# Kernel optimization log

Hardware: AMD Instinct MI355X
Metric: run time of the kernel (lower is better)

The kernel has to match this reference:

```python
import jax, jax.numpy as jnp
import numpy as np

B, S, D, H = 4, 2048, 1024, 16
DK = D // H
NEG = -1.0e9

def setup_inputs() -> dict:
    key = jax.random.key(0)
    ks = jax.random.split(key, 9)
    scale = 1.0 / np.sqrt(D)
    x = jax.random.normal(ks[0], (B, S, D), dtype=jnp.float32)
    # causal mask: positions with mask==0 are filled with -1e9
    mask = jnp.tril(jnp.ones((S, S), dtype=jnp.int32))[None, None]  # [1,1,S,S]
    Wq = jax.random.normal(ks[1], (D, D), dtype=jnp.float32) * scale
    bq = jax.random.normal(ks[2], (D,), dtype=jnp.float32) * 0.01
    Wk = jax.random.normal(ks[3], (D, D), dtype=jnp.float32) * scale
    bk = jax.random.normal(ks[4], (D,), dtype=jnp.float32) * 0.01
    Wv = jax.random.normal(ks[5], (D, D), dtype=jnp.float32) * scale
    bv = jax.random.normal(ks[6], (D,), dtype=jnp.float32) * 0.01
    Wo = jax.random.normal(ks[7], (D, D), dtype=jnp.float32) * scale
    bo = jax.random.normal(ks[8], (D,), dtype=jnp.float32) * 0.01
    return {"x": x, "mask": mask, "Wq": Wq, "bq": bq, "Wk": Wk, "bk": bk,
            "Wv": Wv, "bv": bv, "Wo": Wo, "bo": bo}

def reference(x, mask, Wq, bq, Wk, bk, Wv, bv, Wo, bo):
    Bb, Ss, Dd = x.shape
    q = (x @ Wq.T + bq).reshape(Bb, Ss, H, DK).transpose(0, 2, 1, 3)  # [B,H,S,DK]
    k = (x @ Wk.T + bk).reshape(Bb, Ss, H, DK).transpose(0, 2, 1, 3)
    v = (x @ Wv.T + bv).reshape(Bb, Ss, H, DK).transpose(0, 2, 1, 3)
    scaled = jnp.einsum('bhqd,bhkd->bhqk', q, k) / jnp.sqrt(jnp.float32(DK))
    scaled = jnp.where(mask == 0, jnp.float32(NEG), scaled)
    attn = jax.nn.softmax(scaled, axis=-1)  # dropout prob = 0 -> identity
    vals = jnp.einsum('bhqk,bhkd->bhqd', attn, v)  # [B,H,S,DK]
    vals = vals.transpose(0, 2, 1, 3).reshape(Bb, Ss, H * DK)
    out = vals @ Wo.T + bo
    return out
```

## Files before the change

kernel.cpp:

```cpp
#include <hip/hip_runtime.h>
#include <hip/hip_bf16.h>
#include <cstdint>

#define B_ 4
#define S_ 2048
#define D_ 1024
#define H_ 16
#define DK_ 64

typedef _Float16 h8 __attribute__((ext_vector_type(8)));
typedef _Float16 h4 __attribute__((ext_vector_type(4)));
typedef float f32x4 __attribute__((ext_vector_type(4)));
typedef float f32x16 __attribute__((ext_vector_type(16)));
typedef unsigned int u32x4 __attribute__((ext_vector_type(4)));

__device__ __forceinline__ void gload16(const void* src, void* lds) {
  __builtin_amdgcn_global_load_lds((const __attribute__((address_space(1))) void*)src,
                                   (__attribute__((address_space(3))) void*)lds, 16, 0, 0);
}

__global__ __launch_bounds__(256) void conv_all(
    const float* __restrict__ x,
    const float* __restrict__ Wq, const float* __restrict__ Wk,
    const float* __restrict__ Wv, const float* __restrict__ Wo,
    const float* __restrict__ bq, const float* __restrict__ bk,
    const float* __restrict__ bv,
    _Float16* __restrict__ xb, _Float16* __restrict__ wqkv,
    _Float16* __restrict__ wo, float* __restrict__ bqkv) {
  const int bid = blockIdx.x, tid = threadIdx.x;
  if (bid < 4096) {
    int base = (bid * 256 + tid) * 8;
    h8 o;
#pragma unroll
    for (int j = 0; j < 8; ++j) o[j] = (_Float16)x[base + j];
    *(h8*)(xb + base) = o;
  } else {
    int i = (bid - 4096) * 256 + tid;
    int seg = i >> 17, r = i & 131071;
    const float* src = seg == 0 ? Wq : seg == 1 ? Wk : seg == 2 ? Wv : Wo;
    int base = r * 8;
    h8 o;
#pragma unroll
    for (int j = 0; j < 8; ++j) o[j] = (_Float16)src[base + j];
    if (seg < 3)
      *(h8*)(wqkv + (size_t)seg * 1048576 + base) = o;
    else
      *(h8*)(wo + base) = o;
    if (i < 768) {
      int bsel = i >> 8, k = (i & 255) * 4;
      const float* bs = bsel == 0 ? bq : bsel == 1 ? bk : bv;
      float4 v = *(const float4*)(bs + k);
      *(float4*)(bqkv + bsel * 1024 + k) = v;
    }
  }
}

template <int MODE>
__global__ __launch_bounds__(256, 2) void gemm_nt(const _Float16* __restrict__ A,
                                                  const _Float16* __restrict__ Bw,
                                                  const float* __restrict__ bias,
                                                  void* __restrict__ Cout,
                                                  _Float16* __restrict__ Vt) {
  __shared__ char lds[49152];

  const int tid = threadIdx.x;
  const int w = tid >> 6, lane = tid & 63, g = lane >> 4, c = lane & 15;
  const int wm = w >> 1, wn = w & 1;
  const int bn = blockIdx.x;
  const int bm = blockIdx.y;

  f32x4 acc[8][4] = {};

  const int srow = tid >> 3;
  const int scolsw = ((tid & 7) * 16) ^ ((srow & 7) << 4);
  const char* Ab = (const char*)A + (size_t)bm * 256 * 2048;
  const char* Bb = (const char*)Bw + (size_t)bn * 128 * 2048;
  const char* Asrc[8];
  const char* Bsrc[4];
#pragma unroll
  for (int j = 0; j < 8; ++j)
    Asrc[j] = Ab + (size_t)(j * 32 + srow) * 2048 + scolsw;
#pragma unroll
  for (int j = 0; j < 4; ++j)
    Bsrc[j] = Bb + (size_t)(j * 32 + srow) * 2048 + scolsw;
  char* dstA = lds + w * 1024;
  char* dstB = lds + 32768 + w * 1024;

  for (int k0 = 0; k0 < 2048; k0 += 128) {
    __syncthreads();
#pragma unroll
    for (int j = 0; j < 8; ++j) gload16(Asrc[j] + k0, dstA + j * 4096);
#pragma unroll
    for (int j = 0; j < 4; ++j) gload16(Bsrc[j] + k0, dstB + j * 4096);
    __syncthreads();

#pragma unroll
    for (int kk = 0; kk < 2; ++kk) {
      h8 b[4];
#pragma unroll
      for (int ni = 0; ni < 4; ++ni) {
        int row = wn * 64 + ni * 16 + c;
        int off = row * 128 + kk * 64 + g * 16;
        b[ni] = *(const h8*)(lds + 32768 + (off ^ ((row & 7) << 4)));
      }
      h8 a[8];
#pragma unroll
      for (int mi = 0; mi < 8; ++mi) {
        int row = wm * 128 + mi * 16 + c;
        int off = row * 128 + kk * 64 + g * 16;
        a[mi] = *(const h8*)(lds + (off ^ ((row & 7) << 4)));
      }
      __builtin_amdgcn_s_setprio(1);
#pragma unroll
      for (int mi = 0; mi < 8; ++mi)
#pragma unroll
        for (int ni = 0; ni < 4; ++ni)
          acc[mi][ni] = __builtin_amdgcn_mfma_f32_16x16x32_f16(a[mi], b[ni], acc[mi][ni], 0, 0, 0);
      __builtin_amdgcn_s_setprio(0);
    }
  }

  if (MODE == 0 && bn >= 16) {
#pragma unroll
    for (int mi = 0; mi < 8; ++mi)
#pragma unroll
      for (int ni = 0; ni < 4; ++ni) {
        int m0 = bm * 256 + wm * 128 + mi * 16 + g * 4;
        int n = bn * 128 + wn * 64 + ni * 16 + c;
        float bb = bias[n];
        h4 v4;
#pragma unroll
        for (int r = 0; r < 4; ++r) v4[r] = (_Float16)(acc[mi][ni][r] + bb);
        int bI = m0 >> 11, sI = m0 & 2047;
        int dk = n & 63, hh = (n >> 6) & 15;
        *(h4*)(Vt + (((size_t)(bI * 16 + hh) * 64 + dk) * 2048 + sI)) = v4;
      }
  } else {
#pragma unroll
    for (int mi = 0; mi < 8; ++mi)
#pragma unroll
      for (int ni = 0; ni < 4; ++ni)
#pragma unroll
        for (int r = 0; r < 4; ++r) {
          int m = bm * 256 + wm * 128 + mi * 16 + g * 4 + r;
          int n = bn * 128 + wn * 64 + ni * 16 + c;
          float v = acc[mi][ni][r] + bias[n];
          if (MODE == 0) {
            int which = n >> 10, nn = n & 1023;
            int bI = m >> 11, sI = m & 2047, hI = nn >> 6, dkI = nn & 63;
            ((_Float16*)Cout)[(size_t)which * 8388608 +
                              (((size_t)bI * H_ + hI) * S_ + sI) * DK_ + dkI] = (_Float16)v;
          } else {
            ((float*)Cout)[(size_t)m * D_ + n] = v;
          }
        }
  }
}

__global__ __launch_bounds__(512) void attn_fwd(const _Float16* __restrict__ Q,
                                                const _Float16* __restrict__ K,
                                                const _Float16* __restrict__ Vt,
                                                _Float16* __restrict__ vals) {
  __shared__ char lds[3 * 16384];

  const int tid = threadIdx.x;
  const int w = tid >> 6;
  const int lane = tid & 63;
  const int l31 = lane & 31, hi = lane >> 5;
  const int bid = blockIdx.x;
  const int pi = bid >> 6;
  const int bh = bid & 63;
  const int bI = bh >> 4, hI = bh & 15;

  const char* Qb = (const char*)(Q + (size_t)bh * S_ * DK_);
  const char* Kb = (const char*)(K + (size_t)bh * S_ * DK_);
  const char* Vtb = (const char*)(Vt + (size_t)bh * DK_ * S_);

  auto stage = [&](int sloti, int kv0) {
    char* buf = lds + sloti * 16384;
    gload16(Kb + (size_t)kv0 * 128 + (size_t)lane * 128 + w * 16, buf + w * 1024);
    gload16(Vtb + (size_t)lane * 4096 + (size_t)kv0 * 2 + w * 16, buf + 8192 + w * 1024);
  };

  int rdo[4];
#pragma unroll
  for (int ks = 0; ks < 4; ++ks) rdo[ks] = (ks * 2 + hi) * 1024 + l31 * 16;

  const _Float16 qsc = (_Float16)(0.125f * 1.44269504f);

  for (int phase = 0; phase < 2; ++phase) {
    const int sup = (phase == 0) ? pi : 7 - pi;
    const int qw = sup * 8 + w;
    const int nt = 4 * sup + 4;

    h8 qf[4];
#pragma unroll
    for (int ks = 0; ks < 4; ++ks) {
      h8 v = *(const h8*)(Qb + (size_t)(qw * 32 + l31) * 128 + ks * 32 + hi * 16);
#pragma unroll
      for (int j = 0; j < 8; ++j) v[j] *= qsc;
      qf[ks] = v;
    }

    f32x16 o[2] = {};
    float m_ = -1e30f, l_ = 0.f;

    stage(0, 0);
    stage(1, 64);
    asm volatile("s_waitcnt vmcnt(2)" ::: "memory");
    __builtin_amdgcn_s_barrier();
    asm volatile("" ::: "memory");

    for (int t = 0; t < nt; ++t) {
      const char* ldsb = lds + (t % 3) * 16384;
      if (t + 2 < nt) stage((t + 2) % 3, (t + 2) * 64);

      const int rel = qw - 2 * t;
      if (rel >= 0) {
        const bool have1 = (rel >= 1);

        f32x16 s0 = {}, s1 = {};
#pragma unroll
        for (int ks = 0; ks < 4; ++ks) {
          h8 k0 = *(const h8*)(ldsb + rdo[ks]);
          __builtin_amdgcn_s_setprio(1);
          s0 = __builtin_amdgcn_mfma_f32_32x32x16_f16(k0, qf[ks], s0, 0, 0, 0);
          __builtin_amdgcn_s_setprio(0);
          if (have1) {
            h8 k1 = *(const h8*)(ldsb + rdo[ks] + 512);
            __builtin_amdgcn_s_setprio(1);
            s1 = __builtin_amdgcn_mfma_f32_32x32x16_f16(k1, qf[ks], s1, 0, 0, 0);
            __builtin_amdgcn_s_setprio(0);
          }
        }

        if (rel == 0) {
#pragma unroll
          for (int r = 0; r < 16; ++r) {
            int rowidx = (r & 3) + 8 * (r >> 2) + 4 * hi;
            if (rowidx > l31) s0[r] = -1e30f;
          }
        } else if (rel == 1) {
#pragma unroll
          for (int r = 0; r < 16; ++r) {
            int rowidx = (r & 3) + 8 * (r >> 2) + 4 * hi;
            if (rowidx > l31) s1[r] = -1e30f;
          }
        }

        float t8[8];
#pragma unroll
        for (int j = 0; j < 8; ++j) t8[j] = fmaxf(s0[2 * j], s0[2 * j + 1]);
        if (have1)
#pragma unroll
          for (int j = 0; j < 8; ++j) t8[j] = fmaxf(t8[j], fmaxf(s1[2 * j], s1[2 * j + 1]));
        float t4a = fmaxf(t8[0], t8[1]), t4b = fmaxf(t8[2], t8[3]);
        float t4c = fmaxf(t8[4], t8[5]), t4d = fmaxf(t8[6], t8[7]);
        float pmax = fmaxf(fmaxf(t4a, t4b), fmaxf(t4c, t4d));

        if (!__all(pmax <= m_ + 8.f)) {
          float rm = fmaxf(pmax, __shfl_xor(pmax, 32));
          float mn = fmaxf(m_, rm);
          float al = __builtin_amdgcn_exp2f(m_ - mn);
          m_ = mn;
          l_ *= al;
#pragma unroll
          for (int r = 0; r < 16; ++r) {
            float av = __shfl(al, (r & 3) + 8 * (r >> 2) + 4 * hi);
            o[0][r] *= av;
            o[1][r] *= av;
          }
        }

        unsigned int u0[8], u1[8];
        float rsa = 0.f, rsb = 0.f;
#pragma unroll
        for (int j = 0; j < 8; ++j) {
          float e0 = __builtin_amdgcn_exp2f(s0[2 * j] - m_);
          float e1 = __builtin_amdgcn_exp2f(s0[2 * j + 1] - m_);
          rsa += e0 + e1;
          u0[j] = __builtin_bit_cast(unsigned int, __builtin_amdgcn_cvt_pkrtz(e0, e1));
        }
        if (have1) {
#pragma unroll
          for (int j = 0; j < 8; ++j) {
            float e0 = __builtin_amdgcn_exp2f(s1[2 * j] - m_);
            float e1 = __builtin_amdgcn_exp2f(s1[2 * j + 1] - m_);
            rsb += e0 + e1;
            u1[j] = __builtin_bit_cast(unsigned int, __builtin_amdgcn_cvt_pkrtz(e0, e1));
          }
        }
        l_ += rsa + rsb;

        h8 pa0[2], pa1[2];
#pragma unroll
        for (int b = 0; b < 2; ++b) {
          unsigned int ua = u0[4 * b], ub = u0[4 * b + 1];
          unsigned int uc = u0[4 * b + 2], ud = u0[4 * b + 3];
          unsigned int va = hi ? ua : uc, vb = hi ? ub : ud;
          unsigned int xa = __shfl_xor(va, 32), xb = __shfl_xor(vb, 32);
          u32x4 q = {hi ? xa : ua, hi ? xb : ub, hi ? uc : xa, hi ? ud : xb};
          pa0[b] = __builtin_bit_cast(h8, q);
        }
        if (have1) {
#pragma unroll
          for (int b = 0; b < 2; ++b) {
            unsigned int ua = u1[4 * b], ub = u1[4 * b + 1];
            unsigned int uc = u1[4 * b + 2], ud = u1[4 * b + 3];
            unsigned int va = hi ? ua : uc, vb = hi ? ub : ud;
            unsigned int xa = __shfl_xor(va, 32), xb = __shfl_xor(vb, 32);
            u32x4 q = {hi ? xa : ua, hi ? xb : ub, hi ? uc : xa, hi ? ud : xb};
            pa1[b] = __builtin_bit_cast(h8, q);
          }
        }

#pragma unroll
        for (int x = 0; x < 2; ++x) {
#pragma unroll
          for (int kvs = 0; kvs < 4; ++kvs) {
            int ni = kvs >> 1, b = kvs & 1;
            if (!have1 && ni == 1) continue;
            h8 vf = *(const h8*)(ldsb + 8192 + rdo[kvs] + x * 512);
            h8 pa = ni ? pa1[b] : pa0[b];
            __builtin_amdgcn_s_setprio(1);
            o[x] = __builtin_amdgcn_mfma_f32_32x32x16_f16(pa, vf, o[x], 0, 0, 0);
            __builtin_amdgcn_s_setprio(0);
          }
        }
      }

      if (t + 2 < nt)
        asm volatile("s_waitcnt vmcnt(2)" ::: "memory");
      else
        asm volatile("s_waitcnt vmcnt(0)" ::: "memory");
      __builtin_amdgcn_s_barrier();
      asm volatile("" ::: "memory");
    }

    float lt = l_ + __shfl_xor(l_, 32);
    float linv = 1.0f / lt;
#pragma unroll
    for (int r = 0; r < 16; ++r) {
      int qidx = (r & 3) + 8 * (r >> 2) + 4 * hi;
      float inv = __shfl(linv, qidx);
      int qrow = qw * 32 + qidx;
      size_t rowoff = ((size_t)bI * S_ + qrow) * D_ + hI * 64 + l31;
      vals[rowoff] = (_Float16)(o[0][r] * inv);
      vals[rowoff + 32] = (_Float16)(o[1][r] * inv);
    }
  }
}

extern "C" void kernel_launch(void* const* d_in, const int* in_sizes, int n_in,
                              void* d_out, int out_size, void* d_ws, size_t ws_size,
                              hipStream_t stream) {
  const float* x  = (const float*)d_in[0];
  const float* Wq = (const float*)d_in[2];
  const float* bq = (const float*)d_in[3];
  const float* Wk = (const float*)d_in[4];
  const float* bk = (const float*)d_in[5];
  const float* Wv = (const float*)d_in[6];
  const float* bv = (const float*)d_in[7];
  const float* Wo = (const float*)d_in[8];
  const float* bo = (const float*)d_in[9];
  float* out = (float*)d_out;

  char* ws = (char*)d_ws;
  size_t off = 0;
  auto alloc = [&](size_t bytes) {
    char* p = ws + off;
    off += (bytes + 255) & ~(size_t)255;
    return p;
  };
  _Float16* xb   = (_Float16*)alloc((size_t)B_ * S_ * D_ * 2);
  _Float16* wqkv = (_Float16*)alloc((size_t)3 * D_ * D_ * 2);
  _Float16* wob  = (_Float16*)alloc((size_t)D_ * D_ * 2);
  float*    bqkv = (float*)alloc((size_t)3 * D_ * 4);
  _Float16* qkvw = (_Float16*)alloc((size_t)2 * B_ * H_ * S_ * DK_ * 2);
  _Float16* Vtw  = (_Float16*)alloc((size_t)B_ * H_ * S_ * DK_ * 2);
  _Float16* valw = (_Float16*)alloc((size_t)B_ * S_ * D_ * 2);

  conv_all<<<6144, 256, 0, stream>>>(x, Wq, Wk, Wv, Wo, bq, bk, bv, xb, wqkv, wob, bqkv);

  gemm_nt<0><<<dim3(24, 32), 256, 0, stream>>>(xb, wqkv, bqkv, qkvw, Vtw);

  attn_fwd<<<256, 512, 0, stream>>>(qkvw, qkvw + (size_t)8388608, Vtw, valw);

  gemm_nt<1><<<dim3(8, 32), 256, 0, stream>>>(valw, wob, bo, out, nullptr);
}
```

Before: 188.6 us.

## Split attention into one block per query super-tile and shrink output GEMM tiles

The attention kernel no longer runs two paired query super-tiles inside one block. It launches twice as many blocks, 512 instead of 256, each handling a single super-tile, and issues the heaviest causal tiles first so the scheduler can balance load. The output projection GEMM is templated on the M tile size and now uses 128-row tiles, doubling its grid to 512 blocks so more CUs are busy. The cost is more blocks with shorter work, repeated pipeline prologues, and less B-tile reuse per block.

```diff
diff --git a/kernel.cpp b/kernel.cpp
--- a/kernel.cpp
+++ b/kernel.cpp
@@ -55,13 +55,14 @@
   }
 }
 
-template <int MODE>
+template <int MODE, int MI>
 __global__ __launch_bounds__(256, 2) void gemm_nt(const _Float16* __restrict__ A,
                                                   const _Float16* __restrict__ Bw,
                                                   const float* __restrict__ bias,
                                                   void* __restrict__ Cout,
                                                   _Float16* __restrict__ Vt) {
-  __shared__ char lds[49152];
+  constexpr int ABYTES = MI * 4096;
+  __shared__ char lds[ABYTES + 16384];
 
   const int tid = threadIdx.x;
   const int w = tid >> 6, lane = tid & 63, g = lane >> 4, c = lane & 15;
@@ -69,27 +70,27 @@
   const int bn = blockIdx.x;
   const int bm = blockIdx.y;
 
-  f32x4 acc[8][4] = {};
+  f32x4 acc[MI][4] = {};
 
   const int srow = tid >> 3;
   const int scolsw = ((tid & 7) * 16) ^ ((srow & 7) << 4);
-  const char* Ab = (const char*)A + (size_t)bm * 256 * 2048;
+  const char* Ab = (const char*)A + (size_t)bm * (MI * 32) * 2048;
   const char* Bb = (const char*)Bw + (size_t)bn * 128 * 2048;
-  const char* Asrc[8];
+  const char* Asrc[MI];
   const char* Bsrc[4];
 #pragma unroll
-  for (int j = 0; j < 8; ++j)
+  for (int j = 0; j < MI; ++j)
     Asrc[j] = Ab + (size_t)(j * 32 + srow) * 2048 + scolsw;
 #pragma unroll
   for (int j = 0; j < 4; ++j)
     Bsrc[j] = Bb + (size_t)(j * 32 + srow) * 2048 + scolsw;
   char* dstA = lds + w * 1024;
-  char* dstB = lds + 32768 + w * 1024;
+  char* dstB = lds + ABYTES + w * 1024;
 
   for (int k0 = 0; k0 < 2048; k0 += 128) {
     __syncthreads();
 #pragma unroll
-    for (int j = 0; j < 8; ++j) gload16(Asrc[j] + k0, dstA + j * 4096);
+    for (int j = 0; j < MI; ++j) gload16(Asrc[j] + k0, dstA + j * 4096);
 #pragma unroll
     for (int j = 0; j < 4; ++j) gload16(Bsrc[j] + k0, dstB + j * 4096);
     __syncthreads();
@@ -101,18 +102,18 @@
       for (int ni = 0; ni < 4; ++ni) {
         int row = wn * 64 + ni * 16 + c;
         int off = row * 128 + kk * 64 + g * 16;
-        b[ni] = *(const h8*)(lds + 32768 + (off ^ ((row & 7) << 4)));
-      }
-      h8 a[8];
-#pragma unroll
-      for (int mi = 0; mi < 8; ++mi) {
-        int row = wm * 128 + mi * 16 + c;
+        b[ni] = *(const h8*)(lds + ABYTES + (off ^ ((row & 7) << 4)));
+      }
+      h8 a[MI];
+#pragma unroll
+      for (int mi = 0; mi < MI; ++mi) {
+        int row = wm * (MI * 16) + mi * 16 + c;
         int off = row * 128 + kk * 64 + g * 16;
         a[mi] = *(const h8*)(lds + (off ^ ((row & 7) << 4)));
       }
       __builtin_amdgcn_s_setprio(1);
 #pragma unroll
-      for (int mi = 0; mi < 8; ++mi)
+      for (int mi = 0; mi < MI; ++mi)
 #pragma unroll
         for (int ni = 0; ni < 4; ++ni)
           acc[mi][ni] = __builtin_amdgcn_mfma_f32_16x16x32_f16(a[mi], b[ni], acc[mi][ni], 0, 0, 0);
@@ -122,10 +123,10 @@
 
   if (MODE == 0 && bn >= 16) {
 #pragma unroll
-    for (int mi = 0; mi < 8; ++mi)
+    for (int mi = 0; mi < MI; ++mi)
 #pragma unroll
       for (int ni = 0; ni < 4; ++ni) {
-        int m0 = bm * 256 + wm * 128 + mi * 16 + g * 4;
+        int m0 = bm * (MI * 32) + wm * (MI * 16) + mi * 16 + g * 4;
         int n = bn * 128 + wn * 64 + ni * 16 + c;
         float bb = bias[n];
         h4 v4;
@@ -137,12 +138,12 @@
       }
   } else {
 #pragma unroll
-    for (int mi = 0; mi < 8; ++mi)
+    for (int mi = 0; mi < MI; ++mi)
 #pragma unroll
       for (int ni = 0; ni < 4; ++ni)
 #pragma unroll
         for (int r = 0; r < 4; ++r) {
-          int m = bm * 256 + wm * 128 + mi * 16 + g * 4 + r;
+          int m = bm * (MI * 32) + wm * (MI * 16) + mi * 16 + g * 4 + r;
           int n = bn * 128 + wn * 64 + ni * 16 + c;
           float v = acc[mi][ni][r] + bias[n];
           if (MODE == 0) {
@@ -168,7 +169,8 @@
   const int lane = tid & 63;
   const int l31 = lane & 31, hi = lane >> 5;
   const int bid = blockIdx.x;
-  const int pi = bid >> 6;
+  const int quad = bid >> 6;
+  const int sup = (quad < 4) ? 7 - quad : quad - 4;
   const int bh = bid & 63;
   const int bI = bh >> 4, hI = bh & 15;
 
@@ -188,166 +190,163 @@
 
   const _Float16 qsc = (_Float16)(0.125f * 1.44269504f);
 
-  for (int phase = 0; phase < 2; ++phase) {
-    const int sup = (phase == 0) ? pi : 7 - pi;
-    const int qw = sup * 8 + w;
-    const int nt = 4 * sup + 4;
-
-    h8 qf[4];
-#pragma unroll
-    for (int ks = 0; ks < 4; ++ks) {
-      h8 v = *(const h8*)(Qb + (size_t)(qw * 32 + l31) * 128 + ks * 32 + hi * 16);
-#pragma unroll
-      for (int j = 0; j < 8; ++j) v[j] *= qsc;
-      qf[ks] = v;
-    }
-
-    f32x16 o[2] = {};
-    float m_ = -1e30f, l_ = 0.f;
-
-    stage(0, 0);
-    stage(1, 64);
-    asm volatile("s_waitcnt vmcnt(2)" ::: "memory");
-    __builtin_amdgcn_s_barrier();
-    asm volatile("" ::: "memory");
-
-    for (int t = 0; t < nt; ++t) {
-      const char* ldsb = lds + (t % 3) * 16384;
-      if (t + 2 < nt) stage((t + 2) % 3, (t + 2) * 64);
-
-      const int rel = qw - 2 * t;
-      if (rel >= 0) {
-        const bool have1 = (rel >= 1);
-
-        f32x16 s0 = {}, s1 = {};
-#pragma unroll
-        for (int ks = 0; ks < 4; ++ks) {
-          h8 k0 = *(const h8*)(ldsb + rdo[ks]);
+  const int qw = sup * 8 + w;
+  const int nt = 4 * sup + 4;
+
+  h8 qf[4];
+#pragma unroll
+  for (int ks = 0; ks < 4; ++ks) {
+    h8 v = *(const h8*)(Qb + (size_t)(qw * 32 + l31) * 128 + ks * 32 + hi * 16);
+#pragma unroll
+    for (int j = 0; j < 8; ++j) v[j] *= qsc;
+    qf[ks] = v;
+  }
+
+  f32x16 o[2] = {};
+  float m_ = -1e30f, l_ = 0.f;
+
+  stage(0, 0);
+  stage(1, 64);
+  asm volatile("s_waitcnt vmcnt(2)" ::: "memory");
+  __builtin_amdgcn_s_barrier();
+  asm volatile("" ::: "memory");
+
+  for (int t = 0; t < nt; ++t) {
+    const char* ldsb = lds + (t % 3) * 16384;
+    if (t + 2 < nt) stage((t + 2) % 3, (t + 2) * 64);
+
+    const int rel = qw - 2 * t;
+    if (rel >= 0) {
+      const bool have1 = (rel >= 1);
+
+      f32x16 s0 = {}, s1 = {};
+#pragma unroll
+      for (int ks = 0; ks < 4; ++ks) {
+        h8 k0 = *(const h8*)(ldsb + rdo[ks]);
+        __builtin_amdgcn_s_setprio(1);
+        s0 = __builtin_amdgcn_mfma_f32_32x32x16_f16(k0, qf[ks], s0, 0, 0, 0);
+        __builtin_amdgcn_s_setprio(0);
+        if (have1) {
+          h8 k1 = *(const h8*)(ldsb + rdo[ks] + 512);
           __builtin_amdgcn_s_setprio(1);
-          s0 = __builtin_amdgcn_mfma_f32_32x32x16_f16(k0, qf[ks], s0, 0, 0, 0);
+          s1 = __builtin_amdgcn_mfma_f32_32x32x16_f16(k1, qf[ks], s1, 0, 0, 0);
           __builtin_amdgcn_s_setprio(0);
-          if (have1) {
-            h8 k1 = *(const h8*)(ldsb + rdo[ks] + 512);
-            __builtin_amdgcn_s_setprio(1);
-            s1 = __builtin_amdgcn_mfma_f32_32x32x16_f16(k1, qf[ks], s1, 0, 0, 0);
-            __builtin_amdgcn_s_setprio(0);
-          }
-        }
-
-        if (rel == 0) {
-#pragma unroll
-          for (int r = 0; r < 16; ++r) {
-            int rowidx = (r & 3) + 8 * (r >> 2) + 4 * hi;
-            if (rowidx > l31) s0[r] = -1e30f;
-          }
-        } else if (rel == 1) {
-#pragma unroll
-          for (int r = 0; r < 16; ++r) {
-            int rowidx = (r & 3) + 8 * (r >> 2) + 4 * hi;
-            if (rowidx > l31) s1[r] = -1e30f;
-          }
-        }
-
-        float t8[8];
-#pragma unroll
-        for (int j = 0; j < 8; ++j) t8[j] = fmaxf(s0[2 * j], s0[2 * j + 1]);
-        if (have1)
-#pragma unroll
-          for (int j = 0; j < 8; ++j) t8[j] = fmaxf(t8[j], fmaxf(s1[2 * j], s1[2 * j + 1]));
-        float t4a = fmaxf(t8[0], t8[1]), t4b = fmaxf(t8[2], t8[3]);
-        float t4c = fmaxf(t8[4], t8[5]), t4d = fmaxf(t8[6], t8[7]);
-        float pmax = fmaxf(fmaxf(t4a, t4b), fmaxf(t4c, t4d));
-
-        if (!__all(pmax <= m_ + 8.f)) {
-          float rm = fmaxf(pmax, __shfl_xor(pmax, 32));
-          float mn = fmaxf(m_, rm);
-          float al = __builtin_amdgcn_exp2f(m_ - mn);
-          m_ = mn;
-          l_ *= al;
-#pragma unroll
-          for (int r = 0; r < 16; ++r) {
-            float av = __shfl(al, (r & 3) + 8 * (r >> 2) + 4 * hi);
-            o[0][r] *= av;
-            o[1][r] *= av;
-          }
-        }
-
-        unsigned int u0[8], u1[8];
-        float rsa = 0.f, rsb = 0.f;
+        }
+      }
+
+      if (rel == 0) {
+#pragma unroll
+        for (int r = 0; r < 16; ++r) {
+          int rowidx = (r & 3) + 8 * (r >> 2) + 4 * hi;
+          if (rowidx > l31) s0[r] = -1e30f;
+        }
+      } else if (rel == 1) {
+#pragma unroll
+        for (int r = 0; r < 16; ++r) {
+          int rowidx = (r & 3) + 8 * (r >> 2) + 4 * hi;
+          if (rowidx > l31) s1[r] = -1e30f;
+        }
+      }
+
+      float t8[8];
+#pragma unroll
+      for (int j = 0; j < 8; ++j) t8[j] = fmaxf(s0[2 * j], s0[2 * j + 1]);
+      if (have1)
+#pragma unroll
+        for (int j = 0; j < 8; ++j) t8[j] = fmaxf(t8[j], fmaxf(s1[2 * j], s1[2 * j + 1]));
+      float t4a = fmaxf(t8[0], t8[1]), t4b = fmaxf(t8[2], t8[3]);
+      float t4c = fmaxf(t8[4], t8[5]), t4d = fmaxf(t8[6], t8[7]);
+      float pmax = fmaxf(fmaxf(t4a, t4b), fmaxf(t4c, t4d));
+
+      if (!__all(pmax <= m_ + 8.f)) {
+        float rm = fmaxf(pmax, __shfl_xor(pmax, 32));
+        float mn = fmaxf(m_, rm);
+        float al = __builtin_amdgcn_exp2f(m_ - mn);
+        m_ = mn;
+        l_ *= al;
+#pragma unroll
+        for (int r = 0; r < 16; ++r) {
+          float av = __shfl(al, (r & 3) + 8 * (r >> 2) + 4 * hi);
+          o[0][r] *= av;
+          o[1][r] *= av;
+        }
+      }
+
+      unsigned int u0[8], u1[8];
+      float rsa = 0.f, rsb = 0.f;
+#pragma unroll
+      for (int j = 0; j < 8; ++j) {
+        float e0 = __builtin_amdgcn_exp2f(s0[2 * j] - m_);
+        float e1 = __builtin_amdgcn_exp2f(s0[2 * j + 1] - m_);
+        rsa += e0 + e1;
+        u0[j] = __builtin_bit_cast(unsigned int, __builtin_amdgcn_cvt_pkrtz(e0, e1));
+      }
+      if (have1) {
 #pragma unroll
         for (int j = 0; j < 8; ++j) {
-          float e0 = __builtin_amdgcn_exp2f(s0[2 * j] - m_);
-          float e1 = __builtin_amdgcn_exp2f(s0[2 * j + 1] - m_);
-          rsa += e0 + e1;
-          u0[j] = __builtin_bit_cast(unsigned int, __builtin_amdgcn_cvt_pkrtz(e0, e1));
-        }
-        if (have1) {
-#pragma unroll
-          for (int j = 0; j < 8; ++j) {
-            float e0 = __builtin_amdgcn_exp2f(s1[2 * j] - m_);
-            float e1 = __builtin_amdgcn_exp2f(s1[2 * j + 1] - m_);
-            rsb += e0 + e1;
-            u1[j] = __builtin_bit_cast(unsigned int, __builtin_amdgcn_cvt_pkrtz(e0, e1));
-          }
-        }
-        l_ += rsa + rsb;
-
-        h8 pa0[2], pa1[2];
+          float e0 = __builtin_amdgcn_exp2f(s1[2 * j] - m_);
+          float e1 = __builtin_amdgcn_exp2f(s1[2 * j + 1] - m_);
+          rsb += e0 + e1;
+          u1[j] = __builtin_bit_cast(unsigned int, __builtin_amdgcn_cvt_pkrtz(e0, e1));
+        }
+      }
+      l_ += rsa + rsb;
+
+      h8 pa0[2], pa1[2];
+#pragma unroll
+      for (int b = 0; b < 2; ++b) {
+        unsigned int ua = u0[4 * b], ub = u0[4 * b + 1];
+        unsigned int uc = u0[4 * b + 2], ud = u0[4 * b + 3];
+        unsigned int va = hi ? ua : uc, vb = hi ? ub : ud;
+        unsigned int xa = __shfl_xor(va, 32), xb = __shfl_xor(vb, 32);
+        u32x4 q = {hi ? xa : ua, hi ? xb : ub, hi ? uc : xa, hi ? ud : xb};
+        pa0[b] = __builtin_bit_cast(h8, q);
+      }
+      if (have1) {
 #pragma unroll
         for (int b = 0; b < 2; ++b) {
-          unsigned int ua = u0[4 * b], ub = u0[4 * b + 1];
-          unsigned int uc = u0[4 * b + 2], ud = u0[4 * b + 3];
+          unsigned int ua = u1[4 * b], ub = u1[4 * b + 1];
+          unsigned int uc = u1[4 * b + 2], ud = u1[4 * b + 3];
           unsigned int va = hi ? ua : uc, vb = hi ? ub : ud;
           unsigned int xa = __shfl_xor(va, 32), xb = __shfl_xor(vb, 32);
           u32x4 q = {hi ? xa : ua, hi ? xb : ub, hi ? uc : xa, hi ? ud : xb};
-          pa0[b] = __builtin_bit_cast(h8, q);
-        }
-        if (have1) {
-#pragma unroll
-          for (int b = 0; b < 2; ++b) {
-            unsigned int ua = u1[4 * b], ub = u1[4 * b + 1];
-            unsigned int uc = u1[4 * b + 2], ud = u1[4 * b + 3];
-            unsigned int va = hi ? ua : uc, vb = hi ? ub : ud;
-            unsigned int xa = __shfl_xor(va, 32), xb = __shfl_xor(vb, 32);
-            u32x4 q = {hi ? xa : ua, hi ? xb : ub, hi ? uc : xa, hi ? ud : xb};
-            pa1[b] = __builtin_bit_cast(h8, q);
-          }
-        }
-
-#pragma unroll
-        for (int x = 0; x < 2; ++x) {
-#pragma unroll
-          for (int kvs = 0; kvs < 4; ++kvs) {
-            int ni = kvs >> 1, b = kvs & 1;
-            if (!have1 && ni == 1) continue;
-            h8 vf = *(const h8*)(ldsb + 8192 + rdo[kvs] + x * 512);
-            h8 pa = ni ? pa1[b] : pa0[b];
-            __builtin_amdgcn_s_setprio(1);
-            o[x] = __builtin_amdgcn_mfma_f32_32x32x16_f16(pa, vf, o[x], 0, 0, 0);
-            __builtin_amdgcn_s_setprio(0);
-          }
-        }
-      }
-
-      if (t + 2 < nt)
-        asm volatile("s_waitcnt vmcnt(2)" ::: "memory");
-      else
-        asm volatile("s_waitcnt vmcnt(0)" ::: "memory");
-      __builtin_amdgcn_s_barrier();
-      asm volatile("" ::: "memory");
+          pa1[b] = __builtin_bit_cast(h8, q);
+        }
+      }
+
+#pragma unroll
+      for (int x = 0; x < 2; ++x) {
+#pragma unroll
+        for (int kvs = 0; kvs < 4; ++kvs) {
+          int ni = kvs >> 1, b = kvs & 1;
+          if (!have1 && ni == 1) continue;
+          h8 vf = *(const h8*)(ldsb + 8192 + rdo[kvs] + x * 512);
+          h8 pa = ni ? pa1[b] : pa0[b];
+          __builtin_amdgcn_s_setprio(1);
+          o[x] = __builtin_amdgcn_mfma_f32_32x32x16_f16(pa, vf, o[x], 0, 0, 0);
+          __builtin_amdgcn_s_setprio(0);
+        }
+      }
     }
 
-    float lt = l_ + __shfl_xor(l_, 32);
-    float linv = 1.0f / lt;
-#pragma unroll
-    for (int r = 0; r < 16; ++r) {
-      int qidx = (r & 3) + 8 * (r >> 2) + 4 * hi;
-      float inv = __shfl(linv, qidx);
-      int qrow = qw * 32 + qidx;
-      size_t rowoff = ((size_t)bI * S_ + qrow) * D_ + hI * 64 + l31;
-      vals[rowoff] = (_Float16)(o[0][r] * inv);
-      vals[rowoff + 32] = (_Float16)(o[1][r] * inv);
-    }
+    if (t + 2 < nt)
+      asm volatile("s_waitcnt vmcnt(2)" ::: "memory");
+    else
+      asm volatile("s_waitcnt vmcnt(0)" ::: "memory");
+    __builtin_amdgcn_s_barrier();
+    asm volatile("" ::: "memory");
+  }
+
+  float lt = l_ + __shfl_xor(l_, 32);
+  float linv = 1.0f / lt;
+#pragma unroll
+  for (int r = 0; r < 16; ++r) {
+    int qidx = (r & 3) + 8 * (r >> 2) + 4 * hi;
+    float inv = __shfl(linv, qidx);
+    int qrow = qw * 32 + qidx;
+    size_t rowoff = ((size_t)bI * S_ + qrow) * D_ + hI * 64 + l31;
+    vals[rowoff] = (_Float16)(o[0][r] * inv);
+    vals[rowoff + 32] = (_Float16)(o[1][r] * inv);
   }
 }
 
@@ -382,9 +381,9 @@
 
   conv_all<<<6144, 256, 0, stream>>>(x, Wq, Wk, Wv, Wo, bq, bk, bv, xb, wqkv, wob, bqkv);
 
-  gemm_nt<0><<<dim3(24, 32), 256, 0, stream>>>(xb, wqkv, bqkv, qkvw, Vtw);
-
-  attn_fwd<<<256, 512, 0, stream>>>(qkvw, qkvw + (size_t)8388608, Vtw, valw);
-
-  gemm_nt<1><<<dim3(8, 32), 256, 0, stream>>>(valw, wob, bo, out, nullptr);
-}
+  gemm_nt<0, 8><<<dim3(24, 32), 256, 0, stream>>>(xb, wqkv, bqkv, qkvw, Vtw);
+
+  attn_fwd<<<512, 512, 0, stream>>>(qkvw, qkvw + (size_t)8388608, Vtw, valw);
+
+  gemm_nt<1, 4><<<dim3(8, 64), 256, 0, stream>>>(valw, wob, bo, out, nullptr);
+}
```

Measured after the change: 188.7 us. Within noise of the previous version (+0.0%).

## Double-buffer GEMM LDS tiles and split each tile across 8 waves

Applied to the files above, without the earlier changes.

The GEMM kernel now uses two LDS buffers, so the next K-tile's global-to-LDS loads are issued while the current tile is being computed, with explicit vmcnt waits and barriers. Block size doubles from 256 to 512 threads, with 8 waves each owning a 64x64 sub-tile instead of 4 waves owning 128x64. This aims to hide global load latency and cut per-wave accumulator registers. The cost is twice the LDS (96 KB) and one resident block per CU.

```diff
diff --git a/kernel.cpp b/kernel.cpp
--- a/kernel.cpp
+++ b/kernel.cpp
@@ -56,12 +56,12 @@
 }
 
 template <int MODE>
-__global__ __launch_bounds__(256, 2) void gemm_nt(const _Float16* __restrict__ A,
-                                                  const _Float16* __restrict__ Bw,
-                                                  const float* __restrict__ bias,
-                                                  void* __restrict__ Cout,
-                                                  _Float16* __restrict__ Vt) {
-  __shared__ char lds[49152];
+__global__ __launch_bounds__(512, 1) void gemm_pipe(const _Float16* __restrict__ A,
+                                                    const _Float16* __restrict__ Bw,
+                                                    const float* __restrict__ bias,
+                                                    void* __restrict__ Cout,
+                                                    _Float16* __restrict__ Vt) {
+  __shared__ char lds[2 * 49152];
 
   const int tid = threadIdx.x;
   const int w = tid >> 6, lane = tid & 63, g = lane >> 4, c = lane & 15;
@@ -69,31 +69,43 @@
   const int bn = blockIdx.x;
   const int bm = blockIdx.y;
 
-  f32x4 acc[8][4] = {};
+  f32x4 acc[4][4] = {};
 
   const int srow = tid >> 3;
   const int scolsw = ((tid & 7) * 16) ^ ((srow & 7) << 4);
   const char* Ab = (const char*)A + (size_t)bm * 256 * 2048;
   const char* Bb = (const char*)Bw + (size_t)bn * 128 * 2048;
-  const char* Asrc[8];
-  const char* Bsrc[4];
-#pragma unroll
-  for (int j = 0; j < 8; ++j)
-    Asrc[j] = Ab + (size_t)(j * 32 + srow) * 2048 + scolsw;
+  const char* Asrc[4];
+  const char* Bsrc[2];
 #pragma unroll
   for (int j = 0; j < 4; ++j)
-    Bsrc[j] = Bb + (size_t)(j * 32 + srow) * 2048 + scolsw;
-  char* dstA = lds + w * 1024;
-  char* dstB = lds + 32768 + w * 1024;
-
-  for (int k0 = 0; k0 < 2048; k0 += 128) {
-    __syncthreads();
-#pragma unroll
-    for (int j = 0; j < 8; ++j) gload16(Asrc[j] + k0, dstA + j * 4096);
-#pragma unroll
-    for (int j = 0; j < 4; ++j) gload16(Bsrc[j] + k0, dstB + j * 4096);
-    __syncthreads();
-
+    Asrc[j] = Ab + (size_t)(j * 64 + srow) * 2048 + scolsw;
+#pragma unroll
+  for (int j = 0; j < 2; ++j)
+    Bsrc[j] = Bb + (size_t)(j * 64 + srow) * 2048 + scolsw;
+
+  auto stage = [&](int t) {
+    char* slot = lds + (t & 1) * 49152;
+    const int k0 = t * 128;
+#pragma unroll
+    for (int j = 0; j < 4; ++j) gload16(Asrc[j] + k0, slot + j * 8192 + w * 1024);
+#pragma unroll
+    for (int j = 0; j < 2; ++j) gload16(Bsrc[j] + k0, slot + 32768 + j * 8192 + w * 1024);
+  };
+
+  stage(0);
+
+  for (int t = 0; t < 16; ++t) {
+    if (t < 15) {
+      stage(t + 1);
+      asm volatile("s_waitcnt vmcnt(6)" ::: "memory");
+    } else {
+      asm volatile("s_waitcnt vmcnt(0)" ::: "memory");
+    }
+    __builtin_amdgcn_s_barrier();
+    asm volatile("" ::: "memory");
+
+    const char* slot = lds + (t & 1) * 49152;
 #pragma unroll
     for (int kk = 0; kk < 2; ++kk) {
       h8 b[4];
@@ -101,31 +113,34 @@
       for (int ni = 0; ni < 4; ++ni) {
         int row = wn * 64 + ni * 16 + c;
         int off = row * 128 + kk * 64 + g * 16;
-        b[ni] = *(const h8*)(lds + 32768 + (off ^ ((row & 7) << 4)));
+        b[ni] = *(const h8*)(slot + 32768 + (off ^ ((row & 7) << 4)));
       }
-      h8 a[8];
-#pragma unroll
-      for (int mi = 0; mi < 8; ++mi) {
-        int row = wm * 128 + mi * 16 + c;
+      h8 a[4];
+#pragma unroll
+      for (int mi = 0; mi < 4; ++mi) {
+        int row = wm * 64 + mi * 16 + c;
         int off = row * 128 + kk * 64 + g * 16;
-        a[mi] = *(const h8*)(lds + (off ^ ((row & 7) << 4)));
+        a[mi] = *(const h8*)(slot + (off ^ ((row & 7) << 4)));
       }
       __builtin_amdgcn_s_setprio(1);
 #pragma unroll
-      for (int mi = 0; mi < 8; ++mi)
+      for (int mi = 0; mi < 4; ++mi)
 #pragma unroll
         for (int ni = 0; ni < 4; ++ni)
           acc[mi][ni] = __builtin_amdgcn_mfma_f32_16x16x32_f16(a[mi], b[ni], acc[mi][ni], 0, 0, 0);
       __builtin_amdgcn_s_setprio(0);
     }
+
+    __builtin_amdgcn_s_barrier();
+    asm volatile("" ::: "memory");
   }
 
   if (MODE == 0 && bn >= 16) {
 #pragma unroll
-    for (int mi = 0; mi < 8; ++mi)
+    for (int mi = 0; mi < 4; ++mi)
 #pragma unroll
       for (int ni = 0; ni < 4; ++ni) {
-        int m0 = bm * 256 + wm * 128 + mi * 16 + g * 4;
+        int m0 = bm * 256 + wm * 64 + mi * 16 + g * 4;
         int n = bn * 128 + wn * 64 + ni * 16 + c;
         float bb = bias[n];
         h4 v4;
@@ -137,12 +152,12 @@
       }
   } else {
 #pragma unroll
-    for (int mi = 0; mi < 8; ++mi)
+    for (int mi = 0; mi < 4; ++mi)
 #pragma unroll
       for (int ni = 0; ni < 4; ++ni)
 #pragma unroll
         for (int r = 0; r < 4; ++r) {
-          int m = bm * 256 + wm * 128 + mi * 16 + g * 4 + r;
+          int m = bm * 256 + wm * 64 + mi * 16 + g * 4 + r;
           int n = bn * 128 + wn * 64 + ni * 16 + c;
           float v = acc[mi][ni][r] + bias[n];
           if (MODE == 0) {
@@ -382,9 +397,9 @@
 
   conv_all<<<6144, 256, 0, stream>>>(x, Wq, Wk, Wv, Wo, bq, bk, bv, xb, wqkv, wob, bqkv);
 
-  gemm_nt<0><<<dim3(24, 32), 256, 0, stream>>>(xb, wqkv, bqkv, qkvw, Vtw);
+  gemm_pipe<0><<<dim3(24, 32), 512, 0, stream>>>(xb, wqkv, bqkv, qkvw, Vtw);
 
   attn_fwd<<<256, 512, 0, stream>>>(qkvw, qkvw + (size_t)8388608, Vtw, valw);
 
-  gemm_nt<1><<<dim3(8, 32), 256, 0, stream>>>(valw, wob, bo, out, nullptr);
+  gemm_pipe<1><<<dim3(8, 32), 512, 0, stream>>>(valw, wob, bo, out, nullptr);
 }
```

After: 181.3 us. -3.9%, faster.
